# Kernel optimization log

Measured on AMD Instinct MI355X. Metric: run time of the kernel, lower is better.

## Reference

```python
import jax, jax.numpy as jnp
import numpy as np

B, NF, G, H, W = 4, 64, 8, 96, 96
K, KK = 3, 9
CG = NF // G  # channels per deformable group


def _conv3(x, w, b):
    # 3x3 conv, stride 1, pad 1, NCHW/OIHW
    y = jax.lax.conv_general_dilated(x, w, (1, 1), ((1, 1), (1, 1)),
                                     dimension_numbers=('NCHW', 'OIHW', 'NCHW'))
    return y + b[None, :, None, None]


def _lrelu(x):
    return jnp.where(x >= 0, x, 0.1 * x)


def _up2(x):
    # bilinear x2 upsample, align_corners=False (PyTorch semantics: src clamped at 0, indices clamped at n-1)
    def up_axis(x, axis):
        n = x.shape[axis]
        src = jnp.maximum((jnp.arange(2 * n, dtype=jnp.float32) + 0.5) / 2.0 - 0.5, 0.0)
        i0 = jnp.floor(src).astype(jnp.int32)
        i1 = jnp.minimum(i0 + 1, n - 1)
        t = (src - i0.astype(jnp.float32))
        x0 = jnp.take(x, i0, axis=axis)
        x1 = jnp.take(x, i1, axis=axis)
        shp = [1] * x.ndim
        shp[axis] = 2 * n
        t = t.reshape(shp)
        return x0 * (1.0 - t) + x1 * t
    return up_axis(up_axis(x, 2), 3)


def _dcn(x, off_feat, w_om, b_om, w_d, b_d):
    # Modulated deformable conv (DCNv2, separate offset input), 3x3, stride 1, pad 1, dil 1,
    # conv groups = 1, deformable groups = G.
    b, c, h, w = x.shape
    om = _conv3(off_feat, w_om, b_om)                     # [B, 3*G*KK, H, W]
    o_y, o_x, m = jnp.split(om, 3, axis=1)                # each [B, G*KK, H, W]
    off_y = o_y.reshape(b, G, KK, h, w)
    off_x = o_x.reshape(b, G, KK, h, w)
    mask = jax.nn.sigmoid(m).reshape(b, G, KK, h, w)

    dy = (jnp.arange(KK, dtype=jnp.float32) // K - 1.0)   # [-1,-1,-1,0,0,0,1,1,1]
    dx = (jnp.arange(KK, dtype=jnp.float32) % K - 1.0)
    ys = jnp.arange(h, dtype=jnp.float32)
    xs = jnp.arange(w, dtype=jnp.float32)
    # sampling positions: [B, G, KK, H, W]
    py = off_y + ys[None, None, None, :, None] + dy[None, None, :, None, None]
    px = off_x + xs[None, None, None, None, :] + dx[None, None, :, None, None]

    y0f = jnp.floor(py); x0f = jnp.floor(px)
    ty = py - y0f; tx = px - x0f
    y0 = y0f.astype(jnp.int32); x0 = x0f.astype(jnp.int32)
    y1 = y0 + 1; x1 = x0 + 1

    xg = x.reshape(b, G, CG, h * w)  # per-deformable-group channels

    def samp(iy, ix):
        valid = ((iy >= 0) & (iy < h) & (ix >= 0) & (ix < w)).astype(x.dtype)  # [B,G,KK,H,W]
        idx = jnp.clip(iy, 0, h - 1) * w + jnp.clip(ix, 0, w - 1)
        idxf = idx.reshape(b, G, 1, KK * h * w)
        v = jnp.take_along_axis(xg, jnp.broadcast_to(idxf, (b, G, CG, KK * h * w)), axis=3)
        return v.reshape(b, G, CG, KK, h, w) * valid[:, :, None]

    w00 = ((1 - ty) * (1 - tx))[:, :, None]
    w01 = ((1 - ty) * tx)[:, :, None]
    w10 = (ty * (1 - tx))[:, :, None]
    w11 = (ty * tx)[:, :, None]
    cols = (samp(y0, x0) * w00 + samp(y0, x1) * w01 +
            samp(y1, x0) * w10 + samp(y1, x1) * w11)
    cols = cols * mask[:, :, None]                        # modulation
    cols = cols.reshape(b, c, KK, h, w)
    out = jnp.einsum('bckhw,ock->bohw', cols, w_d.reshape(c, c, KK))
    return out + b_d[None, :, None, None]


def setup_inputs() -> dict:
    key = jax.random.key(0)
    ks = jax.random.split(key, 20)
    s = 0.05
    inp = {
        'src0': jax.random.normal(ks[0], (B, NF, H, W), jnp.float32),
        'src1': jax.random.normal(ks[1], (B, NF, H, W), jnp.float32),
        'last_offset': jax.random.normal(ks[2], (B, NF, H // 2, W // 2), jnp.float32),
        'last_feature': jax.random.normal(ks[3], (B, NF, H // 2, W // 2), jnp.float32),
        'w_off1': jax.random.normal(ks[4], (NF, 2 * NF, 3, 3), jnp.float32) * s,
        'b_off1': jax.random.normal(ks[5], (NF,), jnp.float32) * s,
        'w_off2': jax.random.normal(ks[6], (NF, 2 * NF, 3, 3), jnp.float32) * s,
        'b_off2': jax.random.normal(ks[7], (NF,), jnp.float32) * s,
        'w_off3': jax.random.normal(ks[8], (NF, NF, 3, 3), jnp.float32) * s,
        'b_off3': jax.random.normal(ks[9], (NF,), jnp.float32) * s,
        'w_om': jax.random.normal(ks[10], (3 * G * KK, NF, 3, 3), jnp.float32) * s,
        'b_om': jax.random.normal(ks[11], (3 * G * KK,), jnp.float32) * s,
        'w_dcn': jax.random.normal(ks[12], (NF, NF, 3, 3), jnp.float32) * s,
        'b_dcn': jax.random.normal(ks[13], (NF,), jnp.float32) * s,
        'w_fea': jax.random.normal(ks[14], (NF, 2 * NF, 3, 3), jnp.float32) * s,
        'b_fea': jax.random.normal(ks[15], (NF,), jnp.float32) * s,
    }
    return inp


def reference(src0, src1, last_offset, last_feature,
              w_off1, b_off1, w_off2, b_off2, w_off3, b_off3,
              w_om, b_om, w_dcn, b_dcn, w_fea, b_fea):
    offset = _lrelu(_conv3(jnp.concatenate([src0, src1], axis=1), w_off1, b_off1))
    lo = _up2(last_offset)
    offset = _lrelu(_conv3(jnp.concatenate([offset, lo * 2.0], axis=1), w_off2, b_off2))
    offset = _lrelu(_conv3(offset, w_off3, b_off3))
    feature = _dcn(src0, offset, w_om, b_om, w_dcn, b_dcn)
    lf = _up2(last_feature)
    feature = _conv3(jnp.concatenate([feature, lf], axis=1), w_fea, b_fea)
    feature = _lrelu(feature)
    return (offset, feature)
```

## Files before the change

### kernel.cpp

```cpp
#include <hip/hip_runtime.h>
#include <hip/hip_fp16.h>
#include <math.h>

typedef __attribute__((ext_vector_type(8))) short bf16x8;
typedef __attribute__((ext_vector_type(8))) _Float16 half8;
typedef __attribute__((ext_vector_type(4))) float f32x4;
typedef __attribute__((ext_vector_type(4))) int int4v;

#define GL_LDS16(g, l) __builtin_amdgcn_global_load_lds( \
    (const __attribute__((address_space(1))) void*)(g), \
    (__attribute__((address_space(3))) void*)(l), 16, 0, 0)

__device__ __forceinline__ ushort f2bf(float f) {
    union { float f; unsigned u; } v; v.f = f;
    unsigned r = (v.u + 0x7fffu + ((v.u >> 16) & 1u)) >> 16;
    return (ushort)r;
}
__device__ __forceinline__ float bf2f(ushort h) {
    union { unsigned u; float f; } v; v.u = ((unsigned)h) << 16;
    return v.f;
}

__device__ __forceinline__ void prep_one(const float* __restrict__ w,
        ushort* __restrict__ wp, int u, int Cin, int CoutR, int CoutP) {
    int oc = u % CoutP; int t = u / CoutP;
    int kg = t & 3; t >>= 2;
    int kk = t % 9; int cc = t / 9;
    alignas(16) ushort tmp[8];
    for (int j = 0; j < 8; ++j) {
        int c = cc * 32 + kg * 8 + j;
        float v = (oc < CoutR) ? w[((size_t)oc * Cin + c) * 9 + kk] : 0.f;
        tmp[j] = f2bf(v);
    }
    *(int4v*)(wp + (size_t)u * 8) = *(int4v*)tmp;
}

__global__ __launch_bounds__(256) void pack_combo_k(
        const float* __restrict__ s0, const float* __restrict__ s1,
        const float* __restrict__ lo, const float* __restrict__ lf,
        const float* __restrict__ w1, const float* __restrict__ w2,
        const float* __restrict__ w3, const float* __restrict__ wom,
        const float* __restrict__ wd, const float* __restrict__ wf,
        const float* __restrict__ bom,
        ushort* __restrict__ xin1, ushort* __restrict__ xin2,
        ushort* __restrict__ xin4, ushort* __restrict__ xg1,
        ushort* __restrict__ w1p, ushort* __restrict__ w2p,
        ushort* __restrict__ w3p, ushort* __restrict__ womp,
        ushort* __restrict__ wdp, ushort* __restrict__ wfp,
        float* __restrict__ bpp, float* __restrict__ zg) {
    int b = blockIdx.y;
    int z = blockIdx.z;
    int px = blockIdx.x * 64 + (threadIdx.x & 63);
    int u = threadIdx.x >> 6;
    if (z == 0) {
        for (int half = 0; half < 2; ++half) {
            int cg = u + half * 4;
            float vals[16];
            alignas(16) ushort tmp[16];
            for (int i = 0; i < 16; ++i) {
                int c = cg * 16 + i;
                float v = (c < 64) ? s0[((size_t)(b * 64 + c)) * 9216 + px]
                                   : s1[((size_t)(b * 64 + c - 64)) * 9216 + px];
                vals[i] = v;
                tmp[i] = f2bf(v);
            }
            ushort* dst = xin1 + ((size_t)(b * 9216) + px) * 128 + cg * 16;
            *(int4v*)dst = *(int4v*)&tmp[0];
            *(int4v*)(dst + 8) = *(int4v*)&tmp[8];
            if (half == 0) {
                alignas(16) __half th[16];
                for (int i = 0; i < 16; ++i) th[i] = __float2half(vals[i]);
                ushort* gdst = xg1 + (((size_t)(b * 8 + cg * 2) * 9216) + px) * 8;
                *(int4v*)gdst = *(int4v*)&th[0];
                *(int4v*)(gdst + 9216 * 8) = *(int4v*)&th[8];
            }
        }
    } else if (z < 3) {
        const float* in = (z == 1) ? lo : lf;
        float scale = (z == 1) ? 2.0f : 1.0f;
        ushort* xo = (z == 1) ? xin2 : xin4;
        int y = px / 96, x = px % 96;
        float sy = fmaxf(y * 0.5f - 0.25f, 0.f);
        float sx = fmaxf(x * 0.5f - 0.25f, 0.f);
        int y0 = (int)sy, x0 = (int)sx;
        float ty = sy - (float)y0, tx = sx - (float)x0;
        int y1 = min(y0 + 1, 47), x1 = min(x0 + 1, 47);
        alignas(16) ushort tmp[16];
        for (int i = 0; i < 16; ++i) {
            int c = u * 16 + i;
            const float* p = in + ((size_t)(b * 64 + c)) * 2304;
            float v00 = p[y0 * 48 + x0], v01 = p[y0 * 48 + x1];
            float v10 = p[y1 * 48 + x0], v11 = p[y1 * 48 + x1];
            float v = (v00 * (1.f - tx) + v01 * tx) * (1.f - ty)
                    + (v10 * (1.f - tx) + v11 * tx) * ty;
            tmp[i] = f2bf(v * scale);
        }
        ushort* dst = xo + ((size_t)(b * 9216) + px) * 128 + 64 + u * 16;
        *(int4v*)dst = *(int4v*)&tmp[0];
        *(int4v*)(dst + 8) = *(int4v*)&tmp[8];
    } else {
        int uu = (blockIdx.x + 144 * blockIdx.y) * 256 + threadIdx.x;
        if (uu < 9216) prep_one(w1, w1p, uu, 128, 64, 64);
        else if (uu < 18432) prep_one(w2, w2p, uu - 9216, 128, 64, 64);
        else if (uu < 23040) prep_one(w3, w3p, uu - 18432, 64, 64, 64);
        else if (uu < 43776) {
            int v = uu - 23040;
            int ocp = v % 288; int t = v / 288;
            int kg = t & 3; t >>= 2;
            int kk = t % 9; int cc = t / 9;
            int t3 = ocp & 3, gkkp = ocp >> 2;
            alignas(16) ushort tmp[8];
            for (int j = 0; j < 8; ++j) {
                int c = cc * 32 + kg * 8 + j;
                float vv = (t3 < 3)
                    ? wom[((size_t)(t3 * 72 + gkkp) * 64 + c) * 9 + kk] : 0.f;
                tmp[j] = f2bf(vv);
            }
            *(int4v*)(womp + (size_t)v * 8) = *(int4v*)tmp;
        } else if (uu < 48384) {
            int v = uu - 43776;
            int oc = v & 63; int gkk = v >> 6;
            int g = gkk / 9, kk = gkk % 9;
            alignas(16) __half tmp[8];
            for (int j = 0; j < 8; ++j)
                tmp[j] = __float2half(wd[((size_t)oc * 64 + g * 8 + j) * 9 + kk]);
            *(int4v*)(wdp + (size_t)v * 8) = *(int4v*)tmp;
        } else if (uu < 57600) prep_one(wf, wfp, uu - 48384, 128, 64, 64);
        else if (uu < 57888) {
            int ocp = uu - 57600; int t3 = ocp & 3, gkkp = ocp >> 2;
            bpp[ocp] = (t3 < 3) ? bom[t3 * 72 + gkkp] : 0.f;
        } else if (uu < 57904) zg[uu - 57888] = 0.f;
    }
}

template<int CIN, int MT, int NZ, bool LRELU, bool ST_F32, bool ST_CHL>
__global__ __launch_bounds__(256, 4) void conv_mfma_k(
        const ushort* __restrict__ xin,
        const ushort* __restrict__ wp,
        const float* __restrict__ bias,
        float* __restrict__ outf,
        ushort* __restrict__ chl,
        const ushort* __restrict__ zg,
        int CoutR, int CoutP, int ochs, int ocoff) {
    constexpr int SL = CIN / 64;
    constexpr int OCN = MT * 16;
    __shared__ ushort s_act[SL][7200];

    int tid = threadIdx.x;
    int wv = tid >> 6, ln = tid & 63;
    int l15 = ln & 15, l4 = ln >> 4;

    constexpr int TOTAL = 144 * 4 * NZ;
    constexpr int CHUNK = TOTAL / 8;
    int bid = blockIdx.x;
    int nid = (bid & 7) * CHUNK + (bid >> 3);
    int zc = nid % NZ; int r1 = nid / NZ;
    int tile = r1 % 144; int b = r1 / 144;
    int bx = (tile % 12) * 8, by = (tile / 12) * 8;
    int oc0 = zc * OCN;

    int px_l = wv * 16 + l15;
    int py = px_l >> 3, pxx = px_l & 7;
    int b_base = (py * 10 + pxx) * 72 + l4 * 8;

    const ushort* wlane = wp + ((size_t)l4 * CoutP + oc0 + l15) * 8;

    f32x4 acc[MT];
#pragma unroll
    for (int mt = 0; mt < MT; ++mt) acc[mt] = (f32x4){0.f, 0.f, 0.f, 0.f};

    auto STAGE = [&](int sl, int buf) {
        for (int i = tid; i < 900; i += 256) {
            int p = i / 9, q = i - p * 9;
            int gy = by + (p / 10) - 1, gx = bx + (p % 10) - 1;
            const ushort* src = zg;
            if (q < 8 && (unsigned)gy < 96u && (unsigned)gx < 96u)
                src = xin + ((size_t)(b * 9216 + gy * 96 + gx) * CIN
                             + sl * 64 + q * 8);
            GL_LDS16(src, s_act[buf] + (size_t)i * 8);
        }
    };

    STAGE(0, 0);
    __syncthreads();
#pragma unroll
    for (int sl = 0; sl < SL; ++sl) {
        if (sl + 1 < SL) STAGE(sl + 1, (sl + 1) & 1);
#pragma unroll
        for (int cc2 = 0; cc2 < 2; ++cc2) {
#pragma unroll
            for (int kk = 0; kk < 9; ++kk) {
                bf16x8 bfrag = *(const bf16x8*)(s_act[sl & (SL - 1)] + b_base +
                                   ((kk / 3) * 10 + (kk % 3)) * 72 + cc2 * 32);
#pragma unroll
                for (int mt = 0; mt < MT; ++mt) {
                    bf16x8 af = *(const bf16x8*)(wlane +
                        ((size_t)((sl * 2 + cc2) * 36 + kk * 4) * CoutP + mt * 16) * 8);
                    acc[mt] = __builtin_amdgcn_mfma_f32_16x16x32_bf16(
                        af, bfrag, acc[mt], 0, 0, 0);
                }
            }
        }
        if (sl + 1 < SL) __syncthreads();
    }

    int gy = by + py, gx = bx + pxx;
    size_t pxg = (size_t)b * 9216 + gy * 96 + gx;
#pragma unroll
    for (int mt = 0; mt < MT; ++mt) {
        int ocb = oc0 + mt * 16 + l4 * 4;
        ushort hb[4];
#pragma unroll
        for (int r = 0; r < 4; ++r) {
            int oc = ocb + r;
            float v = acc[mt][r] + ((oc < CoutR) ? bias[oc] : 0.f);
            if (LRELU) v = (v >= 0.f) ? v : 0.1f * v;
            hb[r] = f2bf(v);
            if (ST_F32 && oc < CoutR)
                outf[((size_t)b * CoutR + oc) * 9216 + gy * 96 + gx] = v;
        }
        if (ST_CHL && ocb < CoutR) {
            uint2 pk;
            pk.x = (uint)hb[0] | ((uint)hb[1] << 16);
            pk.y = (uint)hb[2] | ((uint)hb[3] << 16);
            *(uint2*)(chl + pxg * ochs + ocoff + ocb) = pk;
        }
    }
}

__global__ __launch_bounds__(192, 3) void dcn_fused_k(
        const ushort* __restrict__ xoff,
        const ushort* __restrict__ xg1,
        const ushort* __restrict__ womp,
        const float* __restrict__ bpp,
        const ushort* __restrict__ wdp,
        const float* __restrict__ bd, ushort* __restrict__ chl,
        const ushort* __restrict__ zg) {
    __shared__ ushort s_x[3456];
    __shared__ float s_red[2][64][17];
    int tid = threadIdx.x;
    int kq = tid >> 6, ln = tid & 63;
    int l15 = ln & 15, l4 = ln >> 4;
    int bid = blockIdx.x;
    int nid = (bid & 7) * 288 + (bid >> 3);
    int pxb = nid % 576; int b = nid / 576;
    int px0 = pxb * 16;
    int px = px0 + l15;
    int y = px0 / 96, x0 = px0 % 96;
    int xx = x0 + l15;

    for (int i = tid; i < 432; i += 192) {
        int P = i >> 3, s8 = i & 7;
        int q = s8 ^ (P & 7);
        int ry = y - 1 + P / 18, rx = x0 - 1 + P % 18;
        const ushort* src = zg;
        if ((unsigned)ry < 96u && (unsigned)rx < 96u)
            src = xoff + (((size_t)b * 9216 + ry * 96 + rx) * 64 + q * 8);
        GL_LDS16(src, s_x + (size_t)i * 8);
    }
    __syncthreads();

    f32x4 aom[6];
#pragma unroll
    for (int s = 0; s < 6; ++s) aom[s] = (f32x4){0.f, 0.f, 0.f, 0.f};
#pragma unroll
    for (int kk = 0; kk < 9; ++kk) {
        int ky = kk / 3, kx = kk % 3;
#pragma unroll
        for (int cc = 0; cc < 2; ++cc) {
            int P = ky * 18 + l15 + kx;
            int c8 = cc * 4 + l4;
            bf16x8 bfrag = *(const bf16x8*)(s_x +
                ((size_t)(P * 8 + (c8 ^ (P & 7)))) * 8);
#pragma unroll
            for (int s = 0; s < 6; ++s) {
                bf16x8 af = *(const bf16x8*)(womp +
                    ((size_t)(((cc * 9 + kk) * 4 + l4) * 288)
                     + (kq * 6 + s) * 16 + l15) * 8);
                aom[s] = __builtin_amdgcn_mfma_f32_16x16x32_bf16(
                    af, bfrag, aom[s], 0, 0, 0);
            }
        }
    }

    f32x4 acc[4];
#pragma unroll
    for (int mt = 0; mt < 4; ++mt) acc[mt] = (f32x4){0.f, 0.f, 0.f, 0.f};

    int4v Abuf[2][4];
    float cwbuf[2][4];

    auto PREP = [&](int s, int4v* A, float* cw) {
        int st = kq * 6 + s;
        int gkk = st * 4 + l4;
        int g = gkk / 9, kk = gkk - g * 9;
        int bofs = st * 16 + l4 * 4;
        float oy = aom[s][0] + bpp[bofs];
        float ox = aom[s][1] + bpp[bofs + 1];
        float mm = 1.f / (1.f + __expf(-(aom[s][2] + bpp[bofs + 2])));
        float py = oy + (float)(y + kk / 3 - 1);
        float pxf = ox + (float)(xx + kk % 3 - 1);
        float yf = floorf(py), xf = floorf(pxf);
        float fy = py - yf, fx = pxf - xf;
        int iy0 = (int)yf, ix0 = (int)xf;
        int iy1 = iy0 + 1, ix1 = ix0 + 1;
        float vy0 = ((unsigned)iy0 < 96u) ? 1.f : 0.f;
        float vy1 = ((unsigned)iy1 < 96u) ? 1.f : 0.f;
        float vx0 = ((unsigned)ix0 < 96u) ? 1.f : 0.f;
        float vx1 = ((unsigned)ix1 < 96u) ? 1.f : 0.f;
        int r0 = min(max(iy0, 0), 95), r1 = min(max(iy1, 0), 95);
        int lb = min(max(ix0, 0), 94);
        float h0 = (float)min(max(ix0 - lb, 0), 1);
        float h1 = (float)min(max(ix1 - lb, 0), 1);
        float wx0 = (1.f - fx) * vx0, wx1 = fx * vx1;
        float xw0 = wx0 * (1.f - h0) + wx1 * (1.f - h1);
        float xw1 = wx0 * h0 + wx1 * h1;
        float rw0 = (1.f - fy) * vy0 * mm, rw1 = fy * vy1 * mm;
        cw[0] = rw0 * xw0; cw[1] = rw0 * xw1;
        cw[2] = rw1 * xw0; cw[3] = rw1 * xw1;
        const ushort* gp = xg1 + ((size_t)(b * 8 + g) * 9216) * 8;
        const ushort* p0 = gp + ((size_t)(r0 * 96 + lb)) * 8;
        const ushort* p1 = gp + ((size_t)(r1 * 96 + lb)) * 8;
        A[0] = *(const int4v*)p0;
        A[1] = *(const int4v*)(p0 + 8);
        A[2] = *(const int4v*)p1;
        A[3] = *(const int4v*)(p1 + 8);
    };

    PREP(0, Abuf[0], cwbuf[0]);
#pragma unroll
    for (int s = 0; s < 6; ++s) {
        if (s + 1 < 6) PREP(s + 1, Abuf[(s + 1) & 1], cwbuf[(s + 1) & 1]);
        const int4v* A = Abuf[s & 1];
        const float* cw = cwbuf[s & 1];
        union { int4v v; __half2 h2[4]; } a0, a1, b0, b1;
        a0.v = A[0]; a1.v = A[1]; b0.v = A[2]; b1.v = A[3];
        __half2 w0 = __float2half2_rn(cw[0]);
        __half2 w1 = __float2half2_rn(cw[1]);
        __half2 w2 = __float2half2_rn(cw[2]);
        __half2 w3 = __float2half2_rn(cw[3]);
        union { __half2 h2[4]; half8 v; } bu;
#pragma unroll
        for (int j = 0; j < 4; ++j) {
            __half2 t = __hmul2(a0.h2[j], w0);
            t = __hfma2(a1.h2[j], w1, t);
            t = __hfma2(b0.h2[j], w2, t);
            t = __hfma2(b1.h2[j], w3, t);
            bu.h2[j] = t;
        }
        int gkk = (kq * 6 + s) * 4 + l4;
#pragma unroll
        for (int mt = 0; mt < 4; ++mt) {
            half8 af = *(const half8*)(wdp +
                ((size_t)gkk * 64 + mt * 16 + l15) * 8);
            acc[mt] = __builtin_amdgcn_mfma_f32_16x16x32_f16(
                af, bu.v, acc[mt], 0, 0, 0);
        }
    }

    if (kq) {
#pragma unroll
        for (int mt = 0; mt < 4; ++mt)
#pragma unroll
            for (int r = 0; r < 4; ++r)
                s_red[kq - 1][ln][mt * 4 + r] = acc[mt][r];
    }
    __syncthreads();
    if (!kq) {
        size_t pb = (size_t)b * 9216 + px;
#pragma unroll
        for (int mt = 0; mt < 4; ++mt) {
            ushort hb[4];
#pragma unroll
            for (int r = 0; r < 4; ++r) {
                int oc = mt * 16 + l4 * 4 + r;
                float v = acc[mt][r] + s_red[0][ln][mt * 4 + r]
                        + s_red[1][ln][mt * 4 + r] + bd[oc];
                hb[r] = f2bf(v);
            }
            uint2 pk;
            pk.x = (uint)hb[0] | ((uint)hb[1] << 16);
            pk.y = (uint)hb[2] | ((uint)hb[3] << 16);
            *(uint2*)(chl + pb * 128 + mt * 16 + l4 * 4) = pk;
        }
    }
}

extern "C" void kernel_launch(void* const* d_in, const int* in_sizes, int n_in,
                              void* d_out, int out_size, void* d_ws, size_t ws_size,
                              hipStream_t stream) {
    const float* src0  = (const float*)d_in[0];
    const float* src1  = (const float*)d_in[1];
    const float* l_off = (const float*)d_in[2];
    const float* l_fea = (const float*)d_in[3];
    const float* w1 = (const float*)d_in[4];   const float* b1 = (const float*)d_in[5];
    const float* w2 = (const float*)d_in[6];   const float* b2 = (const float*)d_in[7];
    const float* w3 = (const float*)d_in[8];   const float* b3 = (const float*)d_in[9];
    const float* wom = (const float*)d_in[10]; const float* bom = (const float*)d_in[11];
    const float* wd = (const float*)d_in[12];  const float* bd = (const float*)d_in[13];
    const float* wf = (const float*)d_in[14];  const float* bf = (const float*)d_in[15];

    char* W = (char*)d_ws;
    ushort* xin1 = (ushort*)(W + 0);
    ushort* xin2 = (ushort*)(W + 9437184);
    ushort* xoff = (ushort*)(W + 9437184);
    ushort* xin3 = (ushort*)(W + 18874368);
    ushort* xin4 = (ushort*)(W + 44826624);
    ushort* xg1  = (ushort*)(W + 54263808);
    ushort* w1p  = (ushort*)(W + 58982400);
    ushort* w2p  = (ushort*)(W + 59129856);
    ushort* w3p  = (ushort*)(W + 59277312);
    ushort* womp = (ushort*)(W + 59351040);
    ushort* wdp  = (ushort*)(W + 59682816);
    ushort* wfp  = (ushort*)(W + 59756544);
    float*  bpp  = (float*)(W + 59904000);
    float*  zgrd = (float*)(W + 59905152);

    float* out_off = (float*)d_out;
    float* out_fea = out_off + (size_t)4 * 64 * 9216;

    pack_combo_k<<<dim3(144, 4, 4), 256, 0, stream>>>(
        src0, src1, l_off, l_fea, w1, w2, w3, wom, wd, wf, bom,
        xin1, xin2, xin4, xg1, w1p, w2p, w3p, womp, wdp, wfp, bpp, zgrd);

    const ushort* zg = (const ushort*)zgrd;
    conv_mfma_k<128, 2, 2, true, false, true><<<1152, 256, 0, stream>>>(
        xin1, w1p, b1, nullptr, xin2, zg, 64, 64, 128, 0);
    conv_mfma_k<128, 2, 2, true, false, true><<<1152, 256, 0, stream>>>(
        xin2, w2p, b2, nullptr, xin3, zg, 64, 64, 64, 0);
    conv_mfma_k<64, 2, 2, true, true, true><<<1152, 256, 0, stream>>>(
        xin3, w3p, b3, out_off, xoff, zg, 64, 64, 64, 0);
    dcn_fused_k<<<2304, 192, 0, stream>>>(xoff, xg1, womp, bpp, wdp, bd,
                                          xin4, zg);
    conv_mfma_k<128, 2, 2, true, true, false><<<1152, 256, 0, stream>>>(
        xin4, wfp, bf, out_fea, nullptr, zg, 64, 64, 0, 0);
}
```

Before: 133.1 us.

## Interleave offset-conv MFMA with deformable gather in a 3-stage software pipeline

Computes the offset/mask conv accumulator one slot at a time instead of all six up front. Each slot's bilinear gather is issued two iterations before its weighted-sum MFMA runs, using a triple buffer. The goal is to hide global gather latency behind offset-conv MFMA work and to drop the six live aom accumulators. The trade-off is that the shared LDS B-fragments are now reloaded six times, and occupancy is lowered from 3 to 2 to allow more registers.

```diff
diff --git a/kernel.cpp b/kernel.cpp
--- a/kernel.cpp
+++ b/kernel.cpp
@@ -228,7 +228,7 @@
     }
 }
 
-__global__ __launch_bounds__(192, 3) void dcn_fused_k(
+__global__ __launch_bounds__(192, 2) void dcn_fused_k(
         const ushort* __restrict__ xoff,
         const ushort* __restrict__ xg1,
         const ushort* __restrict__ womp,
@@ -260,44 +260,21 @@
     }
     __syncthreads();
 
-    f32x4 aom[6];
-#pragma unroll
-    for (int s = 0; s < 6; ++s) aom[s] = (f32x4){0.f, 0.f, 0.f, 0.f};
-#pragma unroll
-    for (int kk = 0; kk < 9; ++kk) {
-        int ky = kk / 3, kx = kk % 3;
-#pragma unroll
-        for (int cc = 0; cc < 2; ++cc) {
-            int P = ky * 18 + l15 + kx;
-            int c8 = cc * 4 + l4;
-            bf16x8 bfrag = *(const bf16x8*)(s_x +
-                ((size_t)(P * 8 + (c8 ^ (P & 7)))) * 8);
-#pragma unroll
-            for (int s = 0; s < 6; ++s) {
-                bf16x8 af = *(const bf16x8*)(womp +
-                    ((size_t)(((cc * 9 + kk) * 4 + l4) * 288)
-                     + (kq * 6 + s) * 16 + l15) * 8);
-                aom[s] = __builtin_amdgcn_mfma_f32_16x16x32_bf16(
-                    af, bfrag, aom[s], 0, 0, 0);
-            }
-        }
-    }
-
     f32x4 acc[4];
 #pragma unroll
     for (int mt = 0; mt < 4; ++mt) acc[mt] = (f32x4){0.f, 0.f, 0.f, 0.f};
 
-    int4v Abuf[2][4];
-    float cwbuf[2][4];
-
-    auto PREP = [&](int s, int4v* A, float* cw) {
+    int4v Ab[3][4];
+    float cwb[3][4];
+
+    auto PREP = [&](int s, const f32x4& aom, int4v* A, float* cw) {
         int st = kq * 6 + s;
         int gkk = st * 4 + l4;
         int g = gkk / 9, kk = gkk - g * 9;
         int bofs = st * 16 + l4 * 4;
-        float oy = aom[s][0] + bpp[bofs];
-        float ox = aom[s][1] + bpp[bofs + 1];
-        float mm = 1.f / (1.f + __expf(-(aom[s][2] + bpp[bofs + 2])));
+        float oy = aom[0] + bpp[bofs];
+        float ox = aom[1] + bpp[bofs + 1];
+        float mm = 1.f / (1.f + __expf(-(aom[2] + bpp[bofs + 2])));
         float py = oy + (float)(y + kk / 3 - 1);
         float pxf = ox + (float)(xx + kk % 3 - 1);
         float yf = floorf(py), xf = floorf(pxf);
@@ -327,12 +304,7 @@
         A[3] = *(const int4v*)(p1 + 8);
     };
 
-    PREP(0, Abuf[0], cwbuf[0]);
-#pragma unroll
-    for (int s = 0; s < 6; ++s) {
-        if (s + 1 < 6) PREP(s + 1, Abuf[(s + 1) & 1], cwbuf[(s + 1) & 1]);
-        const int4v* A = Abuf[s & 1];
-        const float* cw = cwbuf[s & 1];
+    auto CONSUME = [&](int s, const int4v* A, const float* cw) {
         union { int4v v; __half2 h2[4]; } a0, a1, b0, b1;
         a0.v = A[0]; a1.v = A[1]; b0.v = A[2]; b1.v = A[3];
         __half2 w0 = __float2half2_rn(cw[0]);
@@ -356,6 +328,31 @@
             acc[mt] = __builtin_amdgcn_mfma_f32_16x16x32_f16(
                 af, bu.v, acc[mt], 0, 0, 0);
         }
+    };
+
+#pragma unroll
+    for (int s = 0; s < 8; ++s) {
+        if (s < 6) {
+            f32x4 aom = (f32x4){0.f, 0.f, 0.f, 0.f};
+#pragma unroll
+            for (int kk = 0; kk < 9; ++kk) {
+                int ky = kk / 3, kx = kk % 3;
+#pragma unroll
+                for (int cc = 0; cc < 2; ++cc) {
+                    int P = ky * 18 + l15 + kx;
+                    int c8 = cc * 4 + l4;
+                    bf16x8 bfrag = *(const bf16x8*)(s_x +
+                        ((size_t)(P * 8 + (c8 ^ (P & 7)))) * 8);
+                    bf16x8 af = *(const bf16x8*)(womp +
+                        ((size_t)(((cc * 9 + kk) * 4 + l4) * 288)
+                         + (kq * 6 + s) * 16 + l15) * 8);
+                    aom = __builtin_amdgcn_mfma_f32_16x16x32_bf16(
+                        af, bfrag, aom, 0, 0, 0);
+                }
+            }
+            PREP(s, aom, Ab[s % 3], cwb[s % 3]);
+        }
+        if (s >= 2) CONSUME(s - 2, Ab[(s - 2) % 3], cwb[(s - 2) % 3]);
     }
 
     if (kq) {
```

After: 131.9 us. About the same (-0.9%).
